# Performance work log

Hardware: AMD Instinct MI355X
Metric: run time of the kernel (lower is better)

The kernel has to match this reference:

```python
import jax, jax.numpy as jnp
import numpy as np

# Fixed reactor dimensions and grey-box constants (from hyb_greybox_pars / xuyscales)
NX, NU, NY, NP = 3, 1, 2, 4
NZ = NP * (NY + NU)          # 12
F, V, DELTA = 0.1, 1.0, 1.0
CAMEAN, CBMEAN = 1.0, 0.5    # yscale mean
CASTD, CBSTD = 0.5, 0.3      # yscale std
CAFMEAN, CAFSTD = 2.0, 0.5   # uscale


def _fnn(x, layers):
    """Feed-forward NN: tanh hidden layers, linear output layer."""
    for W, b in layers[:-1]:
        x = jnp.tanh(x @ W + b)
    W, b = layers[-1]
    return x @ W + b


def setup_inputs() -> dict:
    key = jax.random.key(0)
    ks = jax.random.split(key, 16)
    B, T = 2048, 1024
    d = {
        "useq": jax.random.normal(ks[0], (B, T, NU), jnp.float32),
        "x0": 0.1 * jax.random.normal(ks[1], (B, NX + NZ), jnp.float32),
    }
    s1 = 1.0 / np.sqrt(1.0)
    s16 = 1.0 / np.sqrt(16.0)
    s12 = 1.0 / np.sqrt(12.0)
    s32 = 1.0 / np.sqrt(32.0)
    for i, name in enumerate(["r1", "r2", "r3"]):
        d[name + "_W0"] = s1 * jax.random.normal(ks[2 + 2 * i], (1, 16), jnp.float32)
        d[name + "_b0"] = jnp.zeros((16,), jnp.float32)
        d[name + "_W1"] = s16 * jax.random.normal(ks[3 + 2 * i], (16, 1), jnp.float32)
        d[name + "_b1"] = jnp.zeros((1,), jnp.float32)
    d["estC_W0"] = s12 * jax.random.normal(ks[10], (12, 32), jnp.float32)
    d["estC_b0"] = jnp.zeros((32,), jnp.float32)
    d["estC_W1"] = s32 * jax.random.normal(ks[11], (32, 1), jnp.float32)
    d["estC_b1"] = jnp.zeros((1,), jnp.float32)
    return d


def reference(useq, x0,
              r1_W0, r1_b0, r1_W1, r1_b1,
              r2_W0, r2_b0, r2_W1, r2_b1,
              r3_W0, r3_b0, r3_W1, r3_b1,
              estC_W0, estC_b0, estC_W1, estC_b1):
    r1L = [(r1_W0, r1_b0), (r1_W1, r1_b1)]
    r2L = [(r2_W0, r2_b0), (r2_W1, r2_b1)]
    r3L = [(r3_W0, r3_b0), (r3_W1, r3_b1)]
    estCL = [(estC_W0, estC_b0), (estC_W1, estC_b1)]

    def fxu(x, u):
        Ca, Cb, Cc = x[:, 0:1], x[:, 1:2], x[:, 2:3]
        Caf = u[:, 0:1]
        r1 = _fnn(Ca, r1L) * CASTD
        r2 = _fnn(Cb, r2L) * CBSTD
        r3 = _fnn(Cc, r3L) * CBSTD
        Ca = Ca * CASTD + CAMEAN
        Cb = Cb * CBSTD + CBMEAN
        Cc = Cc * CBSTD + CBMEAN
        Caf = Caf * CAFSTD + CAFMEAN
        dCa = F * (Caf - Ca) / V - r1
        dCb = -F * Cb / V + r1 - 3.0 * r2 + r3
        dCc = -F * Cc / V + r2 - r3
        return jnp.concatenate([dCa / CASTD, dCb / CBSTD, dCc / CBSTD], axis=-1)

    def step(xz, u):
        x, z = xz[:, :NX], xz[:, NX:]
        ypseq, upseq = z[:, :NP * NY], z[:, NP * NY:]
        k1 = fxu(x, u)
        k2 = fxu(x + DELTA * (k1 / 2.0), u)
        k3 = fxu(x + DELTA * (k2 / 2.0), u)
        k4 = fxu(x + DELTA * k3, u)
        xplus = x + (DELTA / 6.0) * (k1 + 2.0 * k2 + 2.0 * k3 + k4)
        zplus = jnp.concatenate([ypseq[:, NY:], x[:, :NY], upseq[:, NU:], u], axis=-1)
        CcNN = _fnn(z, estCL)
        y = jnp.concatenate([x, CcNN], axis=-1)   # [B, Ny + 2*numUnmeasGb] = [B, 4]
        return jnp.concatenate([xplus, zplus], axis=-1), y

    u_t = jnp.swapaxes(useq, 0, 1)                # [T, B, Nu]
    _, ys = jax.lax.scan(step, x0, u_t)           # ys: [T, B, 4]
    return jnp.swapaxes(ys, 0, 1)                 # [B, T, 4]
```

## Files before the change

kernel.cpp:

```cpp
#include <hip/hip_runtime.h>

#define TT 1024
#define BB 2048
#define K1 8
#define L2E2 2.8853900817779268f

template <int CTRL>
__device__ __forceinline__ float dpp_add(float x) {
  int y = __builtin_amdgcn_update_dpp(0, __float_as_int(x), CTRL, 0xF, 0xF, true);
  return x + __int_as_float(y);
}
__device__ __forceinline__ float sum16(float x) {
  x = dpp_add<0xB1>(x);
  x = dpp_add<0x4E>(x);
  x = dpp_add<0x141>(x);
  x = dpp_add<0x140>(x);
  return x;
}
__device__ __forceinline__ float rdlane(float x, int l) {
  return __int_as_float(__builtin_amdgcn_readlane(__float_as_int(x), l));
}

__global__ __launch_bounds__(256) void phase1_kernel(
    const float* __restrict__ useq, const float* __restrict__ x0,
    const float* __restrict__ r1W0, const float* __restrict__ r1b0,
    const float* __restrict__ r1W1, const float* __restrict__ r1b1,
    const float* __restrict__ r2W0, const float* __restrict__ r2b0,
    const float* __restrict__ r2W1, const float* __restrict__ r2b1,
    const float* __restrict__ r3W0, const float* __restrict__ r3b0,
    const float* __restrict__ r3W1, const float* __restrict__ r3b1,
    float* __restrict__ out) {
  const int lane = threadIdx.x & 63;
  const int row = lane >> 4;
  const int j = lane & 15;
  const int e =
      __builtin_amdgcn_readfirstlane(blockIdx.x * 4 + (threadIdx.x >> 6));

  const float* W0p = (row == 0) ? r1W0 : (row == 1) ? r2W0 : r3W0;
  const float* b0p = (row == 0) ? r1b0 : (row == 1) ? r2b0 : r3b0;
  const float* W1p = (row == 0) ? r1W1 : (row == 1) ? r2W1 : r3W1;

  const float w0s = W0p[j] * L2E2;
  const float b0s = b0p[j] * L2E2;
  const float wn = -2.0f * W1p[j];

  float C1 = r1b1[0], C2 = r2b1[0], C3 = r3b1[0];
  for (int q = 0; q < 16; ++q) {
    C1 += r1W1[q];
    C2 += r2W1[q];
    C3 += r3W1[q];
  }
  const float caC = 0.2f - C1;
  const float cbC = -1.0f / 6.0f + (5.0f / 3.0f) * C1 - 3.0f * C2 + C3;
  const float ccC = -1.0f / 6.0f + C2 - C3;

  const float cstBase = (row == 0) ? caC : (row == 1) ? cbC : ccC;
  const float uco = (row == 0) ? 0.1f : 0.0f;
  const float a1 = (row == 0) ? -1.0f : (row == 1) ? (5.0f / 3.0f) : 0.0f;
  const float a2 = (row == 1) ? -3.0f : (row == 2) ? 1.0f : 0.0f;
  const float a3 = (row == 1) ? 1.0f : (row == 2) ? -1.0f : 0.0f;

  float S = x0[e * 15 + ((row < 3) ? row : 2)];

  const float* up = useq + e * TT;
  float* op = out + (size_t)e * TT * 4;

#define STAGE(SS, KK)                                                     \
  {                                                                       \
    float rv = __builtin_amdgcn_rcpf(                                     \
        __builtin_amdgcn_exp2f(fmaf(w0s, (SS), b0s)) + 1.0f);             \
    float q = sum16(wn * rv);                                             \
    float P1 = rdlane(q, 0);                                              \
    float P2 = rdlane(q, 16);                                             \
    float P3 = rdlane(q, 32);                                             \
    float t_ = fmaf(-0.1f, (SS), cstS);                                   \
    t_ = fmaf(a1, P1, t_);                                                \
    t_ = fmaf(a2, P2, t_);                                                \
    KK = fmaf(a3, P3, t_);                                                \
  }

#define STEP(UQ, SC_)                                                     \
  {                                                                       \
    const float cstS = fmaf(uco, (UQ), cstBase);                          \
    SC_ = S;                                                              \
    float k1, k2, k3, k4;                                                 \
    STAGE(S, k1)                                                          \
    float s2 = fmaf(0.5f, k1, S);                                         \
    STAGE(s2, k2)                                                         \
    float s3 = fmaf(0.5f, k2, S);                                         \
    STAGE(s3, k3)                                                         \
    float s4 = S + k3;                                                    \
    STAGE(s4, k4)                                                         \
    S = fmaf(1.0f / 6.0f, fmaf(2.0f, k2 + k3, k1) + k4, S);               \
  }

  float uc0, uc1, uc2, uc3, uc4, uc5, uc6, uc7;
  {
    float4 a = *(const float4*)(up);
    float4 b = *(const float4*)(up + 4);
    uc0 = a.x; uc1 = a.y; uc2 = a.z; uc3 = a.w;
    uc4 = b.x; uc5 = b.y; uc6 = b.z; uc7 = b.w;
  }

  for (int t0 = 0; t0 < TT; t0 += K1) {
    const int tn = (t0 + K1 <= TT - K1) ? (t0 + K1) : (TT - K1);
    const float4 na = *(const float4*)(up + tn);
    const float4 nb = *(const float4*)(up + tn + 4);

    float sc0, sc1, sc2, sc3, sc4, sc5, sc6, sc7;
    STEP(uc0, sc0)
    STEP(uc1, sc1)
    STEP(uc2, sc2)
    STEP(uc3, sc3)
    STEP(uc4, sc4)
    STEP(uc5, sc5)
    STEP(uc6, sc6)
    STEP(uc7, sc7)

    if (j == 0 && row < 3) {
      float* p = op + t0 * 4 + row;
      p[0] = sc0;  p[4] = sc1;  p[8] = sc2;  p[12] = sc3;
      p[16] = sc4; p[20] = sc5; p[24] = sc6; p[28] = sc7;
    }

    uc0 = na.x; uc1 = na.y; uc2 = na.z; uc3 = na.w;
    uc4 = nb.x; uc5 = nb.y; uc6 = nb.z; uc7 = nb.w;
  }
#undef STEP
#undef STAGE
}

__global__ __launch_bounds__(256) void phase2_kernel(
    const float* __restrict__ useq, const float* __restrict__ x0,
    const float* __restrict__ W0, const float* __restrict__ b0,
    const float* __restrict__ W1, const float* __restrict__ b1p,
    float* __restrict__ out) {
  __shared__ float4 wrow[32][4];
  for (int idx = threadIdx.x; idx < 512; idx += 256) {
    const int h = idx >> 4, r = idx & 15;
    float v = 0.0f;
    if (r < 12) v = W0[r * 32 + h] * L2E2;
    else if (r == 12) v = b0[h] * L2E2;
    else if (r == 13) v = -2.0f * W1[h];
    ((float*)&wrow[h][0])[r] = v;
  }
  __syncthreads();

  float base = b1p[0];
#pragma unroll
  for (int h = 0; h < 32; ++h) base += W1[h];

  const int b = blockIdx.x;
  const float* xrow = x0 + b * 15;

  float z[4][12];
#pragma unroll
  for (int k = 0; k < 4; ++k) {
    const int t = k * 256 + (int)threadIdx.x;
    const int g = (b << 10) + t;
    if (t >= 4) {
      const float* px = out + (size_t)g * 4;
#pragma unroll
      for (int i = 0; i < 4; ++i) {
        z[k][2 * i] = px[(i - 4) * 4 + 0];
        z[k][2 * i + 1] = px[(i - 4) * 4 + 1];
      }
      const float* pu = useq + g;
#pragma unroll
      for (int i = 0; i < 4; ++i) z[k][8 + i] = pu[i - 4];
    } else {
#pragma unroll
      for (int i = 0; i < 4; ++i) {
        const int s4 = t - 4 + i;
        const float* py = (s4 >= 0) ? (out + ((size_t)(b << 10) + s4) * 4)
                                    : (xrow + 3 + 2 * (i + t));
        z[k][2 * i] = py[0];
        z[k][2 * i + 1] = py[1];
        const float* pu = (s4 >= 0) ? (useq + (b << 10) + s4)
                                    : (xrow + 11 + i + t);
        z[k][8 + i] = pu[0];
      }
    }
  }

  float ov0 = base, ov1 = base, ov2 = base, ov3 = base;
#pragma unroll
  for (int h = 0; h < 32; ++h) {
    const float4 wa = wrow[h][0];
    const float4 wb = wrow[h][1];
    const float4 wc = wrow[h][2];
    const float4 wd = wrow[h][3];
#define ACC(OV, ZZ)                                                       \
  {                                                                       \
    float a = wd.x;                                                       \
    a = fmaf(ZZ[0], wa.x, a);  a = fmaf(ZZ[1], wa.y, a);                  \
    a = fmaf(ZZ[2], wa.z, a);  a = fmaf(ZZ[3], wa.w, a);                  \
    a = fmaf(ZZ[4], wb.x, a);  a = fmaf(ZZ[5], wb.y, a);                  \
    a = fmaf(ZZ[6], wb.z, a);  a = fmaf(ZZ[7], wb.w, a);                  \
    a = fmaf(ZZ[8], wc.x, a);  a = fmaf(ZZ[9], wc.y, a);                  \
    a = fmaf(ZZ[10], wc.z, a); a = fmaf(ZZ[11], wc.w, a);                 \
    const float r = __builtin_amdgcn_rcpf(__builtin_amdgcn_exp2f(a) + 1.0f); \
    OV = fmaf(wd.y, r, OV);                                               \
  }
    ACC(ov0, z[0])
    ACC(ov1, z[1])
    ACC(ov2, z[2])
    ACC(ov3, z[3])
#undef ACC
  }

  const size_t gb = (size_t)(b << 10) + threadIdx.x;
  out[(gb + 0) * 4 + 3] = ov0;
  out[(gb + 256) * 4 + 3] = ov1;
  out[(gb + 512) * 4 + 3] = ov2;
  out[(gb + 768) * 4 + 3] = ov3;
}

extern "C" void kernel_launch(void* const* d_in, const int* in_sizes, int n_in,
                              void* d_out, int out_size, void* d_ws,
                              size_t ws_size, hipStream_t stream) {
  const float* useq = (const float*)d_in[0];
  const float* x0 = (const float*)d_in[1];
  float* out = (float*)d_out;

  phase1_kernel<<<BB / 4, 256, 0, stream>>>(
      useq, x0,
      (const float*)d_in[2], (const float*)d_in[3], (const float*)d_in[4],
      (const float*)d_in[5], (const float*)d_in[6], (const float*)d_in[7],
      (const float*)d_in[8], (const float*)d_in[9], (const float*)d_in[10],
      (const float*)d_in[11], (const float*)d_in[12], (const float*)d_in[13],
      out);

  phase2_kernel<<<BB, 256, 0, stream>>>(
      useq, x0, (const float*)d_in[14], (const float*)d_in[15],
      (const float*)d_in[16], (const float*)d_in[17], out);
}
```

Baseline: 474.9 us.

## Interleave two batch elements per wavefront in RK4 recurrence and vectorize phase2 loads

Each wavefront in phase1 now advances two independent batch elements at once, interleaving their exp/rcp/DPP reductions so the latency of one serial chain can hide behind the other. One readlane per stage is replaced by a DPP row broadcast, with the coupling coefficients rearranged to match, and the grid is halved. Phase2 reads past outputs as float4 instead of scalar loads. The cost is fewer wavefronts in flight and higher register pressure per wave.

Result: no change. 484.2 us (+2.0%).

```diff
diff --git a/kernel.cpp b/kernel.cpp
--- a/kernel.cpp
+++ b/kernel.cpp
@@ -10,12 +10,15 @@
   int y = __builtin_amdgcn_update_dpp(0, __float_as_int(x), CTRL, 0xF, 0xF, true);
   return x + __int_as_float(y);
 }
-__device__ __forceinline__ float sum16(float x) {
-  x = dpp_add<0xB1>(x);
-  x = dpp_add<0x4E>(x);
-  x = dpp_add<0x141>(x);
-  x = dpp_add<0x140>(x);
-  return x;
+__device__ __forceinline__ void sum16x2(float& a, float& b) {
+  a = dpp_add<0xB1>(a);  b = dpp_add<0xB1>(b);
+  a = dpp_add<0x4E>(a);  b = dpp_add<0x4E>(b);
+  a = dpp_add<0x141>(a); b = dpp_add<0x141>(b);
+  a = dpp_add<0x140>(a); b = dpp_add<0x140>(b);
+}
+__device__ __forceinline__ float bcast15(float x) {
+  return __int_as_float(
+      __builtin_amdgcn_update_dpp(0, __float_as_int(x), 0x142, 0xF, 0xF, true));
 }
 __device__ __forceinline__ float rdlane(float x, int l) {
   return __int_as_float(__builtin_amdgcn_readlane(__float_as_int(x), l));
@@ -33,8 +36,9 @@
   const int lane = threadIdx.x & 63;
   const int row = lane >> 4;
   const int j = lane & 15;
-  const int e =
+  const int gw =
       __builtin_amdgcn_readfirstlane(blockIdx.x * 4 + (threadIdx.x >> 6));
+  const int e0 = gw * 2, e1 = e0 + 1;
 
   const float* W0p = (row == 0) ? r1W0 : (row == 1) ? r2W0 : r3W0;
   const float* b0p = (row == 0) ? r1b0 : (row == 1) ? r2b0 : r3b0;
@@ -46,9 +50,7 @@
 
   float C1 = r1b1[0], C2 = r2b1[0], C3 = r3b1[0];
   for (int q = 0; q < 16; ++q) {
-    C1 += r1W1[q];
-    C2 += r2W1[q];
-    C3 += r3W1[q];
+    C1 += r1W1[q]; C2 += r2W1[q]; C3 += r3W1[q];
   }
   const float caC = 0.2f - C1;
   const float cbC = -1.0f / 6.0f + (5.0f / 3.0f) * C1 - 3.0f * C2 + C3;
@@ -56,78 +58,107 @@
 
   const float cstBase = (row == 0) ? caC : (row == 1) ? cbC : ccC;
   const float uco = (row == 0) ? 0.1f : 0.0f;
-  const float a1 = (row == 0) ? -1.0f : (row == 1) ? (5.0f / 3.0f) : 0.0f;
-  const float a2 = (row == 1) ? -3.0f : (row == 2) ? 1.0f : 0.0f;
-  const float a3 = (row == 1) ? 1.0f : (row == 2) ? -1.0f : 0.0f;
-
-  float S = x0[e * 15 + ((row < 3) ? row : 2)];
-
-  const float* up = useq + e * TT;
-  float* op = out + (size_t)e * TT * 4;
-
-#define STAGE(SS, KK)                                                     \
-  {                                                                       \
-    float rv = __builtin_amdgcn_rcpf(                                     \
-        __builtin_amdgcn_exp2f(fmaf(w0s, (SS), b0s)) + 1.0f);             \
-    float q = sum16(wn * rv);                                             \
-    float P1 = rdlane(q, 0);                                              \
-    float P2 = rdlane(q, 16);                                             \
-    float P3 = rdlane(q, 32);                                             \
-    float t_ = fmaf(-0.1f, (SS), cstS);                                   \
-    t_ = fmaf(a1, P1, t_);                                                \
-    t_ = fmaf(a2, P2, t_);                                                \
-    KK = fmaf(a3, P3, t_);                                                \
-  }
-
-#define STEP(UQ, SC_)                                                     \
-  {                                                                       \
-    const float cstS = fmaf(uco, (UQ), cstBase);                          \
-    SC_ = S;                                                              \
-    float k1, k2, k3, k4;                                                 \
-    STAGE(S, k1)                                                          \
-    float s2 = fmaf(0.5f, k1, S);                                         \
-    STAGE(s2, k2)                                                         \
-    float s3 = fmaf(0.5f, k2, S);                                         \
-    STAGE(s3, k3)                                                         \
-    float s4 = S + k3;                                                    \
-    STAGE(s4, k4)                                                         \
-    S = fmaf(1.0f / 6.0f, fmaf(2.0f, k2 + k3, k1) + k4, S);               \
-  }
-
-  float uc0, uc1, uc2, uc3, uc4, uc5, uc6, uc7;
+  const float aOwn = (row == 1) ? -3.0f : (row == 3) ? 0.0f : -1.0f;
+  const float aM = (row == 1) ? (5.0f / 3.0f) : (row == 2) ? 1.0f : 0.0f;
+  const float aR = (row == 1) ? 1.0f : 0.0f;
+
+  float S0 = x0[e0 * 15 + ((row < 3) ? row : 2)];
+  float S1 = x0[e1 * 15 + ((row < 3) ? row : 2)];
+
+  const float* up0 = useq + e0 * TT;
+  const float* up1 = useq + e1 * TT;
+  float* op0 = out + (size_t)e0 * TT * 4;
+  float* op1 = out + (size_t)e1 * TT * 4;
+
+#define STAGE2(X0_, X1_, K0_, K1_)                                       \
+  {                                                                      \
+    float pa0 = fmaf(w0s, (X0_), b0s);                                   \
+    float pa1 = fmaf(w0s, (X1_), b0s);                                   \
+    float ex0 = __builtin_amdgcn_exp2f(pa0);                             \
+    float ex1 = __builtin_amdgcn_exp2f(pa1);                             \
+    float rv0 = __builtin_amdgcn_rcpf(ex0 + 1.0f);                       \
+    float rv1 = __builtin_amdgcn_rcpf(ex1 + 1.0f);                       \
+    float q0 = wn * rv0;                                                 \
+    float q1 = wn * rv1;                                                 \
+    sum16x2(q0, q1);                                                     \
+    float m0 = bcast15(q0);                                              \
+    float m1 = bcast15(q1);                                              \
+    float P30 = rdlane(q0, 32);                                          \
+    float P31 = rdlane(q1, 32);                                          \
+    float t0_ = fmaf(-0.1f, (X0_), cst0);                                \
+    float t1_ = fmaf(-0.1f, (X1_), cst1);                                \
+    t0_ = fmaf(aOwn, q0, t0_);                                           \
+    t1_ = fmaf(aOwn, q1, t1_);                                           \
+    t0_ = fmaf(aM, m0, t0_);                                             \
+    t1_ = fmaf(aM, m1, t1_);                                             \
+    K0_ = fmaf(aR, P30, t0_);                                            \
+    K1_ = fmaf(aR, P31, t1_);                                            \
+  }
+
+#define STEP2(U0_, U1_, SA_, SB_)                                        \
+  {                                                                      \
+    const float cst0 = fmaf(uco, (U0_), cstBase);                        \
+    const float cst1 = fmaf(uco, (U1_), cstBase);                        \
+    SA_ = S0; SB_ = S1;                                                  \
+    float k10, k11, k20, k21, k30, k31, k40, k41;                        \
+    STAGE2(S0, S1, k10, k11)                                             \
+    float n0 = fmaf(0.5f, k10, S0), n1 = fmaf(0.5f, k11, S1);            \
+    STAGE2(n0, n1, k20, k21)                                             \
+    n0 = fmaf(0.5f, k20, S0); n1 = fmaf(0.5f, k21, S1);                  \
+    STAGE2(n0, n1, k30, k31)                                             \
+    n0 = S0 + k30; n1 = S1 + k31;                                        \
+    STAGE2(n0, n1, k40, k41)                                             \
+    S0 = fmaf(1.0f / 6.0f, fmaf(2.0f, k20 + k30, k10) + k40, S0);        \
+    S1 = fmaf(1.0f / 6.0f, fmaf(2.0f, k21 + k31, k11) + k41, S1);        \
+  }
+
+  float ua0, ua1, ua2, ua3, ua4, ua5, ua6, ua7;
+  float ub0, ub1, ub2, ub3, ub4, ub5, ub6, ub7;
   {
-    float4 a = *(const float4*)(up);
-    float4 b = *(const float4*)(up + 4);
-    uc0 = a.x; uc1 = a.y; uc2 = a.z; uc3 = a.w;
-    uc4 = b.x; uc5 = b.y; uc6 = b.z; uc7 = b.w;
+    float4 a = *(const float4*)(up0);
+    float4 b = *(const float4*)(up0 + 4);
+    float4 c = *(const float4*)(up1);
+    float4 d = *(const float4*)(up1 + 4);
+    ua0 = a.x; ua1 = a.y; ua2 = a.z; ua3 = a.w;
+    ua4 = b.x; ua5 = b.y; ua6 = b.z; ua7 = b.w;
+    ub0 = c.x; ub1 = c.y; ub2 = c.z; ub3 = c.w;
+    ub4 = d.x; ub5 = d.y; ub6 = d.z; ub7 = d.w;
   }
 
   for (int t0 = 0; t0 < TT; t0 += K1) {
     const int tn = (t0 + K1 <= TT - K1) ? (t0 + K1) : (TT - K1);
-    const float4 na = *(const float4*)(up + tn);
-    const float4 nb = *(const float4*)(up + tn + 4);
-
-    float sc0, sc1, sc2, sc3, sc4, sc5, sc6, sc7;
-    STEP(uc0, sc0)
-    STEP(uc1, sc1)
-    STEP(uc2, sc2)
-    STEP(uc3, sc3)
-    STEP(uc4, sc4)
-    STEP(uc5, sc5)
-    STEP(uc6, sc6)
-    STEP(uc7, sc7)
+    const float4 na = *(const float4*)(up0 + tn);
+    const float4 nb = *(const float4*)(up0 + tn + 4);
+    const float4 nc = *(const float4*)(up1 + tn);
+    const float4 nd = *(const float4*)(up1 + tn + 4);
+
+    float sA0, sA1, sA2, sA3, sA4, sA5, sA6, sA7;
+    float sB0, sB1, sB2, sB3, sB4, sB5, sB6, sB7;
+    STEP2(ua0, ub0, sA0, sB0)
+    STEP2(ua1, ub1, sA1, sB1)
+    STEP2(ua2, ub2, sA2, sB2)
+    STEP2(ua3, ub3, sA3, sB3)
+    STEP2(ua4, ub4, sA4, sB4)
+    STEP2(ua5, ub5, sA5, sB5)
+    STEP2(ua6, ub6, sA6, sB6)
+    STEP2(ua7, ub7, sA7, sB7)
 
     if (j == 0 && row < 3) {
-      float* p = op + t0 * 4 + row;
-      p[0] = sc0;  p[4] = sc1;  p[8] = sc2;  p[12] = sc3;
-      p[16] = sc4; p[20] = sc5; p[24] = sc6; p[28] = sc7;
+      float* p0 = op0 + t0 * 4 + row;
+      p0[0] = sA0;  p0[4] = sA1;  p0[8] = sA2;  p0[12] = sA3;
+      p0[16] = sA4; p0[20] = sA5; p0[24] = sA6; p0[28] = sA7;
+      float* p1 = op1 + t0 * 4 + row;
+      p1[0] = sB0;  p1[4] = sB1;  p1[8] = sB2;  p1[12] = sB3;
+      p1[16] = sB4; p1[20] = sB5; p1[24] = sB6; p1[28] = sB7;
     }
 
-    uc0 = na.x; uc1 = na.y; uc2 = na.z; uc3 = na.w;
-    uc4 = nb.x; uc5 = nb.y; uc6 = nb.z; uc7 = nb.w;
-  }
-#undef STEP
-#undef STAGE
+    ua0 = na.x; ua1 = na.y; ua2 = na.z; ua3 = na.w;
+    ua4 = nb.x; ua5 = nb.y; ua6 = nb.z; ua7 = nb.w;
+    ub0 = nc.x; ub1 = nc.y; ub2 = nc.z; ub3 = nc.w;
+    ub4 = nd.x; ub5 = nd.y; ub6 = nd.z; ub7 = nd.w;
+  }
+#undef STEP2
+#undef STAGE2
 }
 
 __global__ __launch_bounds__(256) void phase2_kernel(
@@ -159,12 +190,15 @@
     const int t = k * 256 + (int)threadIdx.x;
     const int g = (b << 10) + t;
     if (t >= 4) {
-      const float* px = out + (size_t)g * 4;
-#pragma unroll
-      for (int i = 0; i < 4; ++i) {
-        z[k][2 * i] = px[(i - 4) * 4 + 0];
-        z[k][2 * i + 1] = px[(i - 4) * 4 + 1];
-      }
+      const float* pb = out + (size_t)(g - 4) * 4;
+      const float4 h0 = *(const float4*)(pb);
+      const float4 h1 = *(const float4*)(pb + 4);
+      const float4 h2 = *(const float4*)(pb + 8);
+      const float4 h3 = *(const float4*)(pb + 12);
+      z[k][0] = h0.x; z[k][1] = h0.y;
+      z[k][2] = h1.x; z[k][3] = h1.y;
+      z[k][4] = h2.x; z[k][5] = h2.y;
+      z[k][6] = h3.x; z[k][7] = h3.y;
       const float* pu = useq + g;
 #pragma unroll
       for (int i = 0; i < 4; ++i) z[k][8 + i] = pu[i - 4];
@@ -223,7 +257,7 @@
   const float* x0 = (const float*)d_in[1];
   float* out = (float*)d_out;
 
-  phase1_kernel<<<BB / 4, 256, 0, stream>>>(
+  phase1_kernel<<<BB / 8, 256, 0, stream>>>(
       useq, x0,
       (const float*)d_in[2], (const float*)d_in[3], (const float*)d_in[4],
       (const float*)d_in[5], (const float*)d_in[6], (const float*)d_in[7],
```

## Fuse estimator MLP into recurrence kernel and replace readlanes with DPP row broadcast

Applied to the files above, without the earlier changes.

Folds the second kernel, the 12-to-32 tanh estimator MLP, into the sequential RK4 wavefront kernel. Each wave now evaluates the estimator for its 8 timesteps from register-held sliding windows of past outputs and inputs, with a DPP reduction across the 32 hidden units. This removes the second launch and the re-read of the output buffer. It also replaces two readlanes per RK stage with a DPP row-broadcast of the previous row's sum, trimming the serial critical path. In exchange the serial kernel does extra ALU and transcendental work per step, and it has only 512 waves, so occupancy is low and that work may not be hidden.

Result: slower. 509.0 us (+7.2%).

```diff
diff --git a/kernel.cpp b/kernel.cpp
--- a/kernel.cpp
+++ b/kernel.cpp
@@ -17,11 +17,15 @@
   x = dpp_add<0x140>(x);
   return x;
 }
+__device__ __forceinline__ float bcast15(float x) {
+  return __int_as_float(
+      __builtin_amdgcn_update_dpp(0, __float_as_int(x), 0x142, 0xF, 0xF, true));
+}
 __device__ __forceinline__ float rdlane(float x, int l) {
   return __int_as_float(__builtin_amdgcn_readlane(__float_as_int(x), l));
 }
 
-__global__ __launch_bounds__(256) void phase1_kernel(
+__global__ __launch_bounds__(256) void fused_kernel(
     const float* __restrict__ useq, const float* __restrict__ x0,
     const float* __restrict__ r1W0, const float* __restrict__ r1b0,
     const float* __restrict__ r1W1, const float* __restrict__ r1b1,
@@ -29,6 +33,8 @@
     const float* __restrict__ r2W1, const float* __restrict__ r2b1,
     const float* __restrict__ r3W0, const float* __restrict__ r3b0,
     const float* __restrict__ r3W1, const float* __restrict__ r3b1,
+    const float* __restrict__ eW0, const float* __restrict__ eb0,
+    const float* __restrict__ eW1, const float* __restrict__ eb1,
     float* __restrict__ out) {
   const int lane = threadIdx.x & 63;
   const int row = lane >> 4;
@@ -39,16 +45,13 @@
   const float* W0p = (row == 0) ? r1W0 : (row == 1) ? r2W0 : r3W0;
   const float* b0p = (row == 0) ? r1b0 : (row == 1) ? r2b0 : r3b0;
   const float* W1p = (row == 0) ? r1W1 : (row == 1) ? r2W1 : r3W1;
-
   const float w0s = W0p[j] * L2E2;
   const float b0s = b0p[j] * L2E2;
   const float wn = -2.0f * W1p[j];
 
   float C1 = r1b1[0], C2 = r2b1[0], C3 = r3b1[0];
   for (int q = 0; q < 16; ++q) {
-    C1 += r1W1[q];
-    C2 += r2W1[q];
-    C3 += r3W1[q];
+    C1 += r1W1[q]; C2 += r2W1[q]; C3 += r3W1[q];
   }
   const float caC = 0.2f - C1;
   const float cbC = -1.0f / 6.0f + (5.0f / 3.0f) * C1 - 3.0f * C2 + C3;
@@ -56,11 +59,28 @@
 
   const float cstBase = (row == 0) ? caC : (row == 1) ? cbC : ccC;
   const float uco = (row == 0) ? 0.1f : 0.0f;
-  const float a1 = (row == 0) ? -1.0f : (row == 1) ? (5.0f / 3.0f) : 0.0f;
-  const float a2 = (row == 1) ? -3.0f : (row == 2) ? 1.0f : 0.0f;
-  const float a3 = (row == 1) ? 1.0f : (row == 2) ? -1.0f : 0.0f;
-
-  float S = x0[e * 15 + ((row < 3) ? row : 2)];
+  const float aOwn = (row == 1) ? -3.0f : -1.0f;
+  const float aM1 = (row == 0) ? 0.0f : (row == 1) ? (5.0f / 3.0f) : 1.0f;
+  const float aR = (row == 1) ? 1.0f : 0.0f;
+
+  float S = x0[e * 15 + ((row == 0) ? 0 : (row == 1) ? 1 : 2)];
+
+  const int h = lane & 31;
+  float ew0 = eW0[0 * 32 + h] * L2E2, ew1 = eW0[1 * 32 + h] * L2E2;
+  float ew2 = eW0[2 * 32 + h] * L2E2, ew3 = eW0[3 * 32 + h] * L2E2;
+  float ew4 = eW0[4 * 32 + h] * L2E2, ew5 = eW0[5 * 32 + h] * L2E2;
+  float ew6 = eW0[6 * 32 + h] * L2E2, ew7 = eW0[7 * 32 + h] * L2E2;
+  float ew8 = eW0[8 * 32 + h] * L2E2, ew9 = eW0[9 * 32 + h] * L2E2;
+  float ew10 = eW0[10 * 32 + h] * L2E2, ew11 = eW0[11 * 32 + h] * L2E2;
+  const float ebv = eb0[h] * L2E2;
+  const float ewn = -2.0f * eW1[h];
+  float ebase = eb1[0];
+  for (int q = 0; q < 32; ++q) ebase += eW1[q];
+
+  const float* xz = x0 + e * 15;
+  float wa0 = xz[3], wb0 = xz[4], wa1 = xz[5], wb1 = xz[6];
+  float wa2 = xz[7], wb2 = xz[8], wa3 = xz[9], wb3 = xz[10];
+  float uw0 = xz[11], uw1 = xz[12], uw2 = xz[13], uw3 = xz[14];
 
   const float* up = useq + e * TT;
   float* op = out + (size_t)e * TT * 4;
@@ -70,13 +90,12 @@
     float rv = __builtin_amdgcn_rcpf(                                     \
         __builtin_amdgcn_exp2f(fmaf(w0s, (SS), b0s)) + 1.0f);             \
     float q = sum16(wn * rv);                                             \
-    float P1 = rdlane(q, 0);                                              \
-    float P2 = rdlane(q, 16);                                             \
+    float m1 = bcast15(q);                                                \
     float P3 = rdlane(q, 32);                                             \
     float t_ = fmaf(-0.1f, (SS), cstS);                                   \
-    t_ = fmaf(a1, P1, t_);                                                \
-    t_ = fmaf(a2, P2, t_);                                                \
-    KK = fmaf(a3, P3, t_);                                                \
+    t_ = fmaf(aOwn, q, t_);                                               \
+    t_ = fmaf(aM1, m1, t_);                                               \
+    KK = fmaf(aR, P3, t_);                                                \
   }
 
 #define STEP(UQ, SC_)                                                     \
@@ -94,6 +113,22 @@
     S = fmaf(1.0f / 6.0f, fmaf(2.0f, k2 + k3, k1) + k4, S);               \
   }
 
+#define EPASS(A0, A1, A2, A3, B0, B1, B2, B3, U0, U1, U2, U3, EST)        \
+  {                                                                       \
+    float acc = ebv;                                                      \
+    acc = fmaf((A0), ew0, acc);  acc = fmaf((B0), ew1, acc);              \
+    acc = fmaf((A1), ew2, acc);  acc = fmaf((B1), ew3, acc);              \
+    acc = fmaf((A2), ew4, acc);  acc = fmaf((B2), ew5, acc);              \
+    acc = fmaf((A3), ew6, acc);  acc = fmaf((B3), ew7, acc);              \
+    acc = fmaf((U0), ew8, acc);  acc = fmaf((U1), ew9, acc);              \
+    acc = fmaf((U2), ew10, acc); acc = fmaf((U3), ew11, acc);             \
+    float rv = __builtin_amdgcn_rcpf(__builtin_amdgcn_exp2f(acc) + 1.0f); \
+    float wv = ewn * rv;                                                  \
+    wv = sum16(wv);                                                       \
+    wv = wv + bcast15(wv);     \
+    EST = wv + ebase;                                                     \
+  }
+
   float uc0, uc1, uc2, uc3, uc4, uc5, uc6, uc7;
   {
     float4 a = *(const float4*)(up);
@@ -117,103 +152,48 @@
     STEP(uc6, sc6)
     STEP(uc7, sc7)
 
-    if (j == 0 && row < 3) {
+    const float bA0 = rdlane(sc0, 0), bB0 = rdlane(sc0, 16);
+    const float bA1 = rdlane(sc1, 0), bB1 = rdlane(sc1, 16);
+    const float bA2 = rdlane(sc2, 0), bB2 = rdlane(sc2, 16);
+    const float bA3 = rdlane(sc3, 0), bB3 = rdlane(sc3, 16);
+    const float bA4 = rdlane(sc4, 0), bB4 = rdlane(sc4, 16);
+    const float bA5 = rdlane(sc5, 0), bB5 = rdlane(sc5, 16);
+    const float bA6 = rdlane(sc6, 0), bB6 = rdlane(sc6, 16);
+    const float bA7 = rdlane(sc7, 0), bB7 = rdlane(sc7, 16);
+
+    float est0, est1, est2, est3, est4, est5, est6, est7;
+    EPASS(wa0, wa1, wa2, wa3, wb0, wb1, wb2, wb3, uw0, uw1, uw2, uw3, est0)
+    EPASS(wa1, wa2, wa3, bA0, wb1, wb2, wb3, bB0, uw1, uw2, uw3, uc0, est1)
+    EPASS(wa2, wa3, bA0, bA1, wb2, wb3, bB0, bB1, uw2, uw3, uc0, uc1, est2)
+    EPASS(wa3, bA0, bA1, bA2, wb3, bB0, bB1, bB2, uw3, uc0, uc1, uc2, est3)
+    EPASS(bA0, bA1, bA2, bA3, bB0, bB1, bB2, bB3, uc0, uc1, uc2, uc3, est4)
+    EPASS(bA1, bA2, bA3, bA4, bB1, bB2, bB3, bB4, uc1, uc2, uc3, uc4, est5)
+    EPASS(bA2, bA3, bA4, bA5, bB2, bB3, bB4, bB5, uc2, uc3, uc4, uc5, est6)
+    EPASS(bA3, bA4, bA5, bA6, bB3, bB4, bB5, bB6, uc3, uc4, uc5, uc6, est7)
+
+    if (j == 0) {
       float* p = op + t0 * 4 + row;
-      p[0] = sc0;  p[4] = sc1;  p[8] = sc2;  p[12] = sc3;
-      p[16] = sc4; p[20] = sc5; p[24] = sc6; p[28] = sc7;
+      const bool isE = (row == 3);
+      p[0]  = isE ? est0 : sc0;
+      p[4]  = isE ? est1 : sc1;
+      p[8]  = isE ? est2 : sc2;
+      p[12] = isE ? est3 : sc3;
+      p[16] = isE ? est4 : sc4;
+      p[20] = isE ? est5 : sc5;
+      p[24] = isE ? est6 : sc6;
+      p[28] = isE ? est7 : sc7;
     }
+
+    wa0 = bA4; wa1 = bA5; wa2 = bA6; wa3 = bA7;
+    wb0 = bB4; wb1 = bB5; wb2 = bB6; wb3 = bB7;
+    uw0 = uc4; uw1 = uc5; uw2 = uc6; uw3 = uc7;
 
     uc0 = na.x; uc1 = na.y; uc2 = na.z; uc3 = na.w;
     uc4 = nb.x; uc5 = nb.y; uc6 = nb.z; uc7 = nb.w;
   }
 #undef STEP
 #undef STAGE
-}
-
-__global__ __launch_bounds__(256) void phase2_kernel(
-    const float* __restrict__ useq, const float* __restrict__ x0,
-    const float* __restrict__ W0, const float* __restrict__ b0,
-    const float* __restrict__ W1, const float* __restrict__ b1p,
-    float* __restrict__ out) {
-  __shared__ float4 wrow[32][4];
-  for (int idx = threadIdx.x; idx < 512; idx += 256) {
-    const int h = idx >> 4, r = idx & 15;
-    float v = 0.0f;
-    if (r < 12) v = W0[r * 32 + h] * L2E2;
-    else if (r == 12) v = b0[h] * L2E2;
-    else if (r == 13) v = -2.0f * W1[h];
-    ((float*)&wrow[h][0])[r] = v;
-  }
-  __syncthreads();
-
-  float base = b1p[0];
-#pragma unroll
-  for (int h = 0; h < 32; ++h) base += W1[h];
-
-  const int b = blockIdx.x;
-  const float* xrow = x0 + b * 15;
-
-  float z[4][12];
-#pragma unroll
-  for (int k = 0; k < 4; ++k) {
-    const int t = k * 256 + (int)threadIdx.x;
-    const int g = (b << 10) + t;
-    if (t >= 4) {
-      const float* px = out + (size_t)g * 4;
-#pragma unroll
-      for (int i = 0; i < 4; ++i) {
-        z[k][2 * i] = px[(i - 4) * 4 + 0];
-        z[k][2 * i + 1] = px[(i - 4) * 4 + 1];
-      }
-      const float* pu = useq + g;
-#pragma unroll
-      for (int i = 0; i < 4; ++i) z[k][8 + i] = pu[i - 4];
-    } else {
-#pragma unroll
-      for (int i = 0; i < 4; ++i) {
-        const int s4 = t - 4 + i;
-        const float* py = (s4 >= 0) ? (out + ((size_t)(b << 10) + s4) * 4)
-                                    : (xrow + 3 + 2 * (i + t));
-        z[k][2 * i] = py[0];
-        z[k][2 * i + 1] = py[1];
-        const float* pu = (s4 >= 0) ? (useq + (b << 10) + s4)
-                                    : (xrow + 11 + i + t);
-        z[k][8 + i] = pu[0];
-      }
-    }
-  }
-
-  float ov0 = base, ov1 = base, ov2 = base, ov3 = base;
-#pragma unroll
-  for (int h = 0; h < 32; ++h) {
-    const float4 wa = wrow[h][0];
-    const float4 wb = wrow[h][1];
-    const float4 wc = wrow[h][2];
-    const float4 wd = wrow[h][3];
-#define ACC(OV, ZZ)                                                       \
-  {                                                                       \
-    float a = wd.x;                                                       \
-    a = fmaf(ZZ[0], wa.x, a);  a = fmaf(ZZ[1], wa.y, a);                  \
-    a = fmaf(ZZ[2], wa.z, a);  a = fmaf(ZZ[3], wa.w, a);                  \
-    a = fmaf(ZZ[4], wb.x, a);  a = fmaf(ZZ[5], wb.y, a);                  \
-    a = fmaf(ZZ[6], wb.z, a);  a = fmaf(ZZ[7], wb.w, a);                  \
-    a = fmaf(ZZ[8], wc.x, a);  a = fmaf(ZZ[9], wc.y, a);                  \
-    a = fmaf(ZZ[10], wc.z, a); a = fmaf(ZZ[11], wc.w, a);                 \
-    const float r = __builtin_amdgcn_rcpf(__builtin_amdgcn_exp2f(a) + 1.0f); \
-    OV = fmaf(wd.y, r, OV);                                               \
-  }
-    ACC(ov0, z[0])
-    ACC(ov1, z[1])
-    ACC(ov2, z[2])
-    ACC(ov3, z[3])
-#undef ACC
-  }
-
-  const size_t gb = (size_t)(b << 10) + threadIdx.x;
-  out[(gb + 0) * 4 + 3] = ov0;
-  out[(gb + 256) * 4 + 3] = ov1;
-  out[(gb + 512) * 4 + 3] = ov2;
-  out[(gb + 768) * 4 + 3] = ov3;
+#undef EPASS
 }
 
 extern "C" void kernel_launch(void* const* d_in, const int* in_sizes, int n_in,
@@ -223,15 +203,12 @@
   const float* x0 = (const float*)d_in[1];
   float* out = (float*)d_out;
 
-  phase1_kernel<<<BB / 4, 256, 0, stream>>>(
+  fused_kernel<<<BB / 4, 256, 0, stream>>>(
       useq, x0,
       (const float*)d_in[2], (const float*)d_in[3], (const float*)d_in[4],
       (const float*)d_in[5], (const float*)d_in[6], (const float*)d_in[7],
       (const float*)d_in[8], (const float*)d_in[9], (const float*)d_in[10],
       (const float*)d_in[11], (const float*)d_in[12], (const float*)d_in[13],
-      out);
-
-  phase2_kernel<<<BB, 256, 0, stream>>>(
-      useq, x0, (const float*)d_in[14], (const float*)d_in[15],
-      (const float*)d_in[16], (const float*)d_in[17], out);
-}
+      (const float*)d_in[14], (const float*)d_in[15], (const float*)d_in[16],
+      (const float*)d_in[17], out);
+}
```
